# Kernel tuning notes

Hardware: AMD Instinct MI355X
Metric: run time of the kernel (lower is better)

The kernel has to match this reference:

```python
import jax, jax.numpy as jnp
import numpy as np

BETA = 4.0  # temperature of soft cluster assignment in filling loss


def _pairwise_sq_dist(a, b):
    # a: [N,D], b: [K,D] -> [N,K] squared euclidean distances
    return (jnp.sum(a * a, -1, keepdims=True)
            - 2.0 * (a @ b.T)
            + jnp.sum(b * b, -1)[None, :])


def setup_inputs() -> dict:
    key = jax.random.key(0)
    k1, k2, k3, k4 = jax.random.split(key, 4)
    N, D, K = 131072, 64, 16
    x = jax.random.normal(k1, (N, D), jnp.float32)
    cluster_centers = jax.random.normal(k2, (K, D), jnp.float32)
    target = jax.random.normal(k3, (N, D), jnp.float32)
    ft = jax.random.uniform(k4, (K,), jnp.float32)
    filling_target = ft / ft.sum()
    # prediction = kmeans assignment of the fixed target set (computed once, constant)
    prediction = jnp.argmin(_pairwise_sq_dist(target, cluster_centers), axis=-1)
    return {"x": x, "cluster_centers": cluster_centers,
            "filling_target": filling_target, "target": target,
            "prediction": prediction}


def reference(x, cluster_centers, filling_target, target, prediction):
    N, D = x.shape
    Nt = target.shape[0]
    K = cluster_centers.shape[0]
    BIG = jnp.finfo(x.dtype).max  # padding value that sorts to the end

    d2 = _pairwise_sq_dist(x, cluster_centers)  # [N,K]

    # --- cluster filling MSE: soft assignment fractions vs filling_target ---
    soft = jax.nn.softmax(-BETA * d2, axis=-1)          # [N,K]
    filling = soft.mean(axis=0)                          # [K]
    loss_fil = jnp.mean((filling - filling_target) ** 2)

    # --- per-cluster sorted (per-dimension 1D) Wasserstein distance ---
    pred_x = jax.lax.stop_gradient(jnp.argmin(d2, axis=-1))  # kmeans_predict(x).detach()
    L = min(N, Nt)  # static upper bound on per-cluster min_size
    rows = jnp.arange(L)

    loss_med = jnp.zeros((), x.dtype)
    for k in range(K):  # fixed structural loop over clusters
        mx = pred_x == k
        mt = prediction == k
        m = jnp.minimum(mx.sum(), mt.sum())  # min_size (dynamic value, static shapes)
        # keep only the FIRST m members (original order), as x[in_cluster][:m]
        keep_x = mx & ((jnp.cumsum(mx) - 1) < m)
        keep_t = mt & ((jnp.cumsum(mt) - 1) < m)
        # mask out non-members with BIG so they sort to the bottom, sort per dim
        xs = jnp.sort(jnp.where(keep_x[:, None], x, BIG), axis=0)[:L]       # [L,D]
        ts = jnp.sort(jnp.where(keep_t[:, None], target, BIG), axis=0)[:L]  # [L,D]
        valid = (rows < m)[:, None]                                          # [L,1]
        diff = jnp.where(valid, jnp.abs(xs - ts), 0.0)
        # mean(|sort(x) - sort(y)|) over the m x D selected elements
        denom = (m * D).astype(x.dtype)
        loss_med = loss_med + jnp.where(m > 0, diff.sum() / denom, 0.0)

    return loss_fil + loss_med
```

## Files before the change

### kernel.cpp

```cpp
#include <hip/hip_runtime.h>
#include <stdint.h>

#define N_ROWS 131072
#define DIMS 64
#define KCL 16
#define BETA 4.0f
#define NBLK 512
#define CHUNK 16384
#define STH 1024
#define SEG_STRIDE 263168
#define VOFF (1u<<21)

typedef unsigned long long u64;
typedef unsigned int u32;

__device__ __forceinline__ u32 enc_f(float f) {
  u32 u = __float_as_uint(f);
  return (u & 0x80000000u) ? ~u : (u | 0x80000000u);
}
__device__ __forceinline__ float dec_f(u32 e) {
  u32 u = (e & 0x80000000u) ? (e & 0x7FFFFFFFu) : ~e;
  return __uint_as_float(u);
}
__device__ __forceinline__ u32 U4(u32 u) { return u ^ ((u >> 3) & 7u); }

#define CS(a,b,dd) { u32 _mn = min(a,b), _mx = max(a,b); a = (dd)?_mn:_mx; b = (dd)?_mx:_mn; }
#define CSV(A,B,D) { CS(A.x,B.x,D) CS(A.y,B.y,D) CS(A.z,B.z,D) CS(A.w,B.w,D) }

#define M16G(a,b,c,d,e,f,g,h,i2,j2,k2,l,m,n,o,p,D) \
  CS(a,i2,D) CS(b,j2,D) CS(c,k2,D) CS(d,l,D) CS(e,m,D) CS(f,n,D) CS(g,o,D) CS(h,p,D) \
  CS(a,e,D)  CS(b,f,D)  CS(c,g,D)  CS(d,h,D) CS(i2,m,D) CS(j2,n,D) CS(k2,o,D) CS(l,p,D) \
  CS(a,c,D)  CS(b,d,D)  CS(e,g,D)  CS(f,h,D) CS(i2,k2,D) CS(j2,l,D) CS(m,o,D) CS(n,p,D) \
  CS(a,b,D)  CS(c,d,D)  CS(e,f,D)  CS(g,h,D) CS(i2,j2,D) CS(k2,l,D) CS(m,n,D) CS(o,p,D)

#define SORT16G(a,b,c,d,e,f,g,h,i2,j2,k2,l,m,n,o,p,D) \
  CS(a,b,D) CS(c,d,!(D)) CS(e,f,D) CS(g,h,!(D)) CS(i2,j2,D) CS(k2,l,!(D)) CS(m,n,D) CS(o,p,!(D)) \
  CS(a,c,D) CS(b,d,D) CS(e,g,!(D)) CS(f,h,!(D)) CS(i2,k2,D) CS(j2,l,D) CS(m,o,!(D)) CS(n,p,!(D)) \
  CS(a,b,D) CS(c,d,D) CS(e,f,!(D)) CS(g,h,!(D)) CS(i2,j2,D) CS(k2,l,D) CS(m,n,!(D)) CS(o,p,!(D)) \
  CS(a,e,D) CS(b,f,D) CS(c,g,D) CS(d,h,D) CS(i2,m,!(D)) CS(j2,n,!(D)) CS(k2,o,!(D)) CS(l,p,!(D)) \
  CS(a,c,D) CS(b,d,D) CS(e,g,D) CS(f,h,D) CS(i2,k2,!(D)) CS(j2,l,!(D)) CS(m,o,!(D)) CS(n,p,!(D)) \
  CS(a,b,D) CS(c,d,D) CS(e,f,D) CS(g,h,D) CS(i2,j2,!(D)) CS(k2,l,!(D)) CS(m,n,!(D)) CS(o,p,!(D)) \
  M16G(a,b,c,d,e,f,g,h,i2,j2,k2,l,m,n,o,p,D)

#define MERGE16F(D) M16G(r0,r1,r2,r3,r4,r5,r6,r7,r8,r9,r10,r11,r12,r13,r14,r15,D)
#define SORT16F(D)  SORT16G(r0,r1,r2,r3,r4,r5,r6,r7,r8,r9,r10,r11,r12,r13,r14,r15,D)

#define LOADTILE16(src) \
  { uint4 _a0=src[U4(ub+0)],_a1=src[U4(ub+1)],_a2=src[U4(ub+2)],_a3=src[U4(ub+3)]; \
    r0=_a0.x;r1=_a0.y;r2=_a0.z;r3=_a0.w; r4=_a1.x;r5=_a1.y;r6=_a1.z;r7=_a1.w; \
    r8=_a2.x;r9=_a2.y;r10=_a2.z;r11=_a2.w; r12=_a3.x;r13=_a3.y;r14=_a3.z;r15=_a3.w; }

#define STORETILE16(dst) \
  { dst[U4(ub+0)]=make_uint4(r0,r1,r2,r3);   dst[U4(ub+1)]=make_uint4(r4,r5,r6,r7); \
    dst[U4(ub+2)]=make_uint4(r8,r9,r10,r11); dst[U4(ub+3)]=make_uint4(r12,r13,r14,r15); }

__device__ __forceinline__ void wave_tail(uint4* lds4, u32 RU, u32 Lw, u32 gbase,
                                          u32 k, u32 jtop, u32 lane)
{
  u32 j = jtop;
  while (j >= 32u) {
    u32 ud = j >> 3;
    if (lane < (Lw >> 4)) {
      u32 bu = RU + (((lane & ~(ud - 1u)) << 2) | (lane & (ud - 1u)));
      bool up = (((gbase + (bu << 2)) & k) == 0u);
      uint4 A0 = lds4[U4(bu)],           A1 = lds4[U4(bu + ud)],
            A2 = lds4[U4(bu + 2u * ud)], A3 = lds4[U4(bu + 3u * ud)];
      CSV(A0,A2,up) CSV(A1,A3,up)
      CSV(A0,A1,up) CSV(A2,A3,up)
      lds4[U4(bu)] = A0;           lds4[U4(bu + ud)] = A1;
      lds4[U4(bu + 2u * ud)] = A2; lds4[U4(bu + 3u * ud)] = A3;
    }
    j >>= 2;
  }
  if (j == 16u) {
    u32 total = Lw >> 3;
    for (u32 inst = lane; inst < total; inst += 64u) {
      u32 bu = RU + (((inst & ~3u) << 1) | (inst & 3u));
      bool up = (((gbase + (bu << 2)) & k) == 0u);
      uint4 A = lds4[U4(bu)], B = lds4[U4(bu + 4u)];
      CSV(A,B,up)
      lds4[U4(bu)] = A; lds4[U4(bu + 4u)] = B;
    }
  }
}

__device__ __forceinline__ void cross1(uint4* lds4, u32 Wn, u32 gb, u32 k, u32 jtop, u32 tid)
{
  u32 ud = jtop >> 2;
  u32 total = Wn >> 3;
  for (u32 inst = tid; inst < total; inst += STH) {
    u32 bu = ((inst & ~(ud - 1u)) << 1) | (inst & (ud - 1u));
    bool up = (((gb + (bu << 2)) & k) == 0u);
    uint4 A = lds4[U4(bu)], B = lds4[U4(bu + ud)];
    CSV(A,B,up)
    lds4[U4(bu)] = A; lds4[U4(bu + ud)] = B;
  }
}
__device__ __forceinline__ void cross2(uint4* lds4, u32 Wn, u32 gb, u32 k, u32 jtop, u32 tid)
{
  u32 ud = jtop >> 3;
  u32 total = Wn >> 4;
  for (u32 inst = tid; inst < total; inst += STH) {
    u32 bu = ((inst & ~(ud - 1u)) << 2) | (inst & (ud - 1u));
    bool up = (((gb + (bu << 2)) & k) == 0u);
    uint4 A0 = lds4[U4(bu)],            A1 = lds4[U4(bu + ud)],
          A2 = lds4[U4(bu + 2u * ud)],  A3 = lds4[U4(bu + 3u * ud)];
    CSV(A0,A2,up) CSV(A1,A3,up)
    CSV(A0,A1,up) CSV(A2,A3,up)
    lds4[U4(bu)] = A0;           lds4[U4(bu + ud)] = A1;
    lds4[U4(bu + 2u * ud)] = A2; lds4[U4(bu + 3u * ud)] = A3;
  }
}
__device__ __forceinline__ void cross3(uint4* lds4, u32 Wn, u32 gb, u32 k, u32 jtop, u32 tid)
{
  u32 ud = jtop >> 4;
  u32 total = Wn >> 5;
  for (u32 inst = tid; inst < total; inst += STH) {
    u32 bu = ((inst & ~(ud - 1u)) << 3) | (inst & (ud - 1u));
    bool up = (((gb + (bu << 2)) & k) == 0u);
    uint4 A0 = lds4[U4(bu)],            A1 = lds4[U4(bu + ud)],
          A2 = lds4[U4(bu + 2u * ud)],  A3 = lds4[U4(bu + 3u * ud)],
          A4 = lds4[U4(bu + 4u * ud)],  A5 = lds4[U4(bu + 5u * ud)],
          A6 = lds4[U4(bu + 6u * ud)],  A7 = lds4[U4(bu + 7u * ud)];
    CSV(A0,A4,up) CSV(A1,A5,up) CSV(A2,A6,up) CSV(A3,A7,up)
    CSV(A0,A2,up) CSV(A1,A3,up) CSV(A4,A6,up) CSV(A5,A7,up)
    CSV(A0,A1,up) CSV(A2,A3,up) CSV(A4,A5,up) CSV(A6,A7,up)
    lds4[U4(bu)] = A0;           lds4[U4(bu + ud)] = A1;
    lds4[U4(bu + 2u * ud)] = A2; lds4[U4(bu + 3u * ud)] = A3;
    lds4[U4(bu + 4u * ud)] = A4; lds4[U4(bu + 5u * ud)] = A5;
    lds4[U4(bu + 6u * ud)] = A6; lds4[U4(bu + 7u * ud)] = A7;
  }
}

__global__ __launch_bounds__(256) void k_assign(
    const float* __restrict__ x, const float* __restrict__ centers,
    const int* __restrict__ predT, int* __restrict__ predX,
    float* __restrict__ fill_sum, u32* __restrict__ histX, u32* __restrict__ histT)
{
  __shared__ float c[KCL][DIMS];
  __shared__ float cn[KCL];
  __shared__ float fs[KCL];
  __shared__ u32 hx[KCL], ht[KCL];
  int tid = threadIdx.x;
  for (int t = tid; t < KCL * DIMS; t += 256) c[t / DIMS][t % DIMS] = centers[t];
  if (tid < KCL) { fs[tid] = 0.f; hx[tid] = 0; ht[tid] = 0; }
  __syncthreads();
  if (tid < KCL) {
    float s = 0.f;
    for (int d = 0; d < DIMS; ++d) s += c[tid][d] * c[tid][d];
    cn[tid] = s;
  }
  __syncthreads();
  int i = blockIdx.x * 256 + tid;
  const float4* xr = (const float4*)(x + (size_t)i * DIMS);
  float dot[KCL];
#pragma unroll
  for (int k = 0; k < KCL; ++k) dot[k] = 0.f;
  for (int t = 0; t < DIMS / 4; ++t) {
    float4 v = xr[t];
#pragma unroll
    for (int k = 0; k < KCL; ++k)
      dot[k] += v.x * c[k][4 * t] + v.y * c[k][4 * t + 1] + v.z * c[k][4 * t + 2] + v.w * c[k][4 * t + 3];
  }
  float sc[KCL];
  float smin = 3.0e38f; int kmin = 0;
#pragma unroll
  for (int k = 0; k < KCL; ++k) {
    sc[k] = cn[k] - 2.f * dot[k];
    if (sc[k] < smin) { smin = sc[k]; kmin = k; }
  }
  float e[KCL]; float esum = 0.f;
#pragma unroll
  for (int k = 0; k < KCL; ++k) { e[k] = expf(-BETA * (sc[k] - smin)); esum += e[k]; }
  float inv = 1.f / esum;
#pragma unroll
  for (int k = 0; k < KCL; ++k) atomicAdd(&fs[k], e[k] * inv);
  predX[i] = kmin;
  atomicAdd(&hx[kmin], 1u);
  atomicAdd(&ht[predT[i]], 1u);
  __syncthreads();
  if (tid < KCL) {
    histX[blockIdx.x * KCL + tid] = hx[tid];
    histT[blockIdx.x * KCL + tid] = ht[tid];
    atomicAdd(&fill_sum[tid], fs[tid]);
  }
}

__global__ __launch_bounds__(512) void k_scan(
    const u32* __restrict__ histX, const u32* __restrict__ histT,
    u32* __restrict__ baseX, u32* __restrict__ baseT,
    const float* __restrict__ fill_sum, const float* __restrict__ ftarget,
    int* __restrict__ m_out, float* __restrict__ w_out,
    int* __restrict__ p_out, int* __restrict__ pOff_out, int* __restrict__ mOff_out,
    int* __restrict__ nlo_out, float* __restrict__ loss_fil)
{
  __shared__ u32 part[2][KCL][17];
  __shared__ u32 tot[2][KCL];
  __shared__ float sq[KCL];
  __shared__ int sp[KCL];
  __shared__ int smv[KCL];
  int tid = threadIdx.x;
  int side = tid >> 8;
  int rem = tid & 255;
  int c = rem >> 4;
  int sub = rem & 15;
  const u32* hist = side ? histT : histX;
  u32* base = side ? baseT : baseX;
  int b0 = sub * 32;
  u32 s = 0;
  for (int b = b0; b < b0 + 32; ++b) s += hist[b * KCL + c];
  part[side][c][sub] = s;
  __syncthreads();
  if (sub == 0) {
    u32 run = 0;
    for (int t = 0; t < 16; ++t) { u32 v = part[side][c][t]; part[side][c][t] = run; run += v; }
    tot[side][c] = run;
  }
  __syncthreads();
  u32 run = part[side][c][sub];
  for (int b = b0; b < b0 + 32; ++b) { base[b * KCL + c] = run; run += hist[b * KCL + c]; }
  if (tid < KCL) {
    int m = min((int)tot[0][tid], (int)tot[1][tid]);
    m_out[tid] = m;
    smv[tid] = m;
    w_out[tid] = (m > 0) ? 1.f / ((float)m * (float)DIMS) : 0.f;
    int pp = 32;
    while (pp < m) pp <<= 1;
    sp[tid] = pp;
    p_out[tid] = pp;
    int nlo = 0;
    if (pp > CHUNK) {
      int nch = pp / CHUNK;
      for (int j = 1; j < nch; j += 2) {
        int v = m - j * CHUNK;
        if (v < 0) v = 0;
        if (v > CHUNK) v = CHUNK;
        nlo += CHUNK - v;
      }
    }
    nlo_out[tid] = nlo;
    float d = fill_sum[tid] / (float)N_ROWS - ftarget[tid];
    sq[tid] = d * d;
  }
  __syncthreads();
  if (tid == 0) {
    float s2 = 0.f;
    int acc = 0, macc = 0;
    for (int k = 0; k < KCL; ++k) {
      s2 += sq[k];
      pOff_out[k] = acc;
      acc += sp[k];
      mOff_out[k] = macc;
      macc += smv[k];
    }
    pOff_out[KCL] = acc;
    mOff_out[KCL] = macc;
    *loss_fil = s2 / (float)KCL;
  }
}

__global__ __launch_bounds__(256) void k_rank(
    const int* __restrict__ predX, const int* __restrict__ predT,
    const u32* __restrict__ baseX, const u32* __restrict__ baseT,
    const int* __restrict__ mG, const int* __restrict__ mOffG,
    int* __restrict__ idxX, int* __restrict__ idxT)
{
  __shared__ int wcX[4][KCL], wcT[4][KCL];
  __shared__ int smo[KCL], sm2[KCL];
  int tid = threadIdx.x;
  int lane = tid & 63, wave = tid >> 6;
  if (tid < KCL) { smo[tid] = mOffG[tid]; sm2[tid] = mG[tid]; }
  int i = blockIdx.x * 256 + tid;
  int kx = predX[i], kt = predT[i];
  u64 below = (1ull << lane) - 1ull;
  int lrX = 0, lrT = 0;
  for (int cc = 0; cc < KCL; ++cc) {
    u64 mx = __ballot(kx == cc);
    u64 mt = __ballot(kt == cc);
    if (kx == cc) lrX = __popcll(mx & below);
    if (kt == cc) lrT = __popcll(mt & below);
    if (lane == 0) { wcX[wave][cc] = __popcll(mx); wcT[wave][cc] = __popcll(mt); }
  }
  __syncthreads();
  int wbX = 0, wbT = 0;
  for (int w2 = 0; w2 < wave; ++w2) { wbX += wcX[w2][kx]; wbT += wcT[w2][kt]; }
  int rX = (int)baseX[blockIdx.x * KCL + kx] + wbX + lrX;
  int rT = (int)baseT[blockIdx.x * KCL + kt] + wbT + lrT;
  if (rX < sm2[kx]) idxX[smo[kx] + rX] = i;
  if (rT < sm2[kt]) idxT[smo[kt] + rT] = i;
}

__global__ __launch_bounds__(256) void k_gather(
    const float* __restrict__ x, const float* __restrict__ tgt,
    const int* __restrict__ idxX, const int* __restrict__ idxT,
    const int* __restrict__ pOffG, const int* __restrict__ mOffG,
    const int* __restrict__ mG, const int* __restrict__ pG,
    u32* __restrict__ valX, u32* __restrict__ valT, int d0, int Dbc)
{
  __shared__ int spOff[KCL + 1];
  __shared__ int smo[KCL], sm2[KCL], sp2[KCL];
  int tid = threadIdx.x;
  if (tid <= KCL) spOff[tid] = pOffG[tid];
  if (tid < KCL) { smo[tid] = mOffG[tid]; sm2[tid] = mG[tid]; sp2[tid] = pG[tid]; }
  __syncthreads();
  int pos = blockIdx.x * 256 + tid;
  if (pos >= spOff[KCL]) return;
  int c = 0;
#pragma unroll
  for (int cc = 1; cc < KCL; ++cc) c += (pos >= spOff[cc]) ? 1 : 0;
  int rel = pos - spOff[c];
  u32* dx = valX + pos;
  u32* dt = valT + pos;
  if (rel < sm2[c]) {
    int w = smo[c] + rel;
    int iX = idxX[w], iT = idxT[w];
    if ((Dbc & 3) == 0) {
      const float4* xr = (const float4*)(x + (size_t)iX * DIMS + d0);
      const float4* tr = (const float4*)(tgt + (size_t)iT * DIMS + d0);
      for (int q = 0; q < (Dbc >> 2); ++q) {
        float4 a = xr[q];
        float4 b = tr[q];
        size_t base = (size_t)(4 * q) * SEG_STRIDE;
        dx[base]                  = enc_f(a.x);
        dx[base + SEG_STRIDE]     = enc_f(a.y);
        dx[base + 2 * (size_t)SEG_STRIDE] = enc_f(a.z);
        dx[base + 3 * (size_t)SEG_STRIDE] = enc_f(a.w);
        dt[base]                  = enc_f(b.x);
        dt[base + SEG_STRIDE]     = enc_f(b.y);
        dt[base + 2 * (size_t)SEG_STRIDE] = enc_f(b.z);
        dt[base + 3 * (size_t)SEG_STRIDE] = enc_f(b.w);
      }
    } else {
      const float* xr = x + (size_t)iX * DIMS + d0;
      const float* tr = tgt + (size_t)iT * DIMS + d0;
      for (int d = 0; d < Dbc; ++d) {
        dx[(size_t)d * SEG_STRIDE] = enc_f(xr[d]);
        dt[(size_t)d * SEG_STRIDE] = enc_f(tr[d]);
      }
    }
  } else {
    u32 pv = (sp2[c] > CHUNK && ((rel >> 14) & 1)) ? 0u : 0xFFFFFFFFu;
    for (int d = 0; d < Dbc; ++d) {
      dx[(size_t)d * SEG_STRIDE] = pv;
      dt[(size_t)d * SEG_STRIDE] = pv;
    }
  }
}

__global__ __launch_bounds__(STH, 8) void k_sort(
    u32* __restrict__ vbase, const int* __restrict__ pG, const int* __restrict__ pOffG,
    const int* __restrict__ mG)
{
  __shared__ __align__(16) u32 lds[CHUNK];
  uint4* lds4 = (uint4*)lds;
  int t = blockIdx.x, c = -1, sub = 0, acc = 0;
  for (int cc = 0; cc < KCL; ++cc) {
    int pc0 = pG[cc];
    int nc = (pc0 > CHUNK) ? (pc0 / CHUNK) : 1;
    if (t < acc + nc) { c = cc; sub = t - acc; break; }
    acc += nc;
  }
  if (c < 0) return;
  int pc = pG[c];
  u32 CH = (u32)min(pc, CHUNK);
  u32 gb = (u32)sub * (u32)CHUNK;
  int v = mG[c] - (int)gb;
  if (v > (int)CH) v = (int)CH;
  if (v <= 0) return;
  u32 W = 32u;
  while (W < (u32)v) W <<= 1;
  if (W > CH) W = CH;
  bool desc = (pc > CHUNK) && (sub & 1);
  u32 inv = desc ? 0xFFFFFFFFu : 0u;
  u32* seg = vbase + (size_t)blockIdx.y * SEG_STRIDE + pOffG[c] + gb;
  uint4* gp4 = (uint4*)seg;
  u32 tid = threadIdx.x;
  u32 lane = tid & 63u;
  u32 wv = tid >> 6;
  u32 ub = tid << 2;
  u32 bas = tid << 4;
  bool act = (bas < W);
  u32 RU = wv << 8;
  u32 runBase = wv << 10;
  bool wact = (runBase < W);
  u32 Lw = W - runBase; if (Lw > 1024u) Lw = 1024u;
  u32 r0,r1,r2,r3,r4,r5,r6,r7,r8,r9,r10,r11,r12,r13,r14,r15;

  if (act) {
    uint4 a0 = gp4[ub + 0], a1 = gp4[ub + 1], a2 = gp4[ub + 2], a3 = gp4[ub + 3];
    r0 = a0.x^inv; r1 = a0.y^inv; r2  = a0.z^inv; r3  = a0.w^inv;
    r4 = a1.x^inv; r5 = a1.y^inv; r6  = a1.z^inv; r7  = a1.w^inv;
    r8 = a2.x^inv; r9 = a2.y^inv; r10 = a2.z^inv; r11 = a2.w^inv;
    r12 = a3.x^inv; r13 = a3.y^inv; r14 = a3.z^inv; r15 = a3.w^inv;
    bool D = ((bas & 16u) == 0u);
    SORT16F(D);
    STORETILE16(lds4);
  }
  if (wact) {
    for (u32 k = 32u; k <= Lw; k <<= 1) {
      wave_tail(lds4, RU, Lw, 0u, k, k >> 1, lane);
      if (act) {
        LOADTILE16(lds4);
        bool D = ((bas & k) == 0u);
        MERGE16F(D);
        if (k < W) { STORETILE16(lds4); }
        else {
          gp4[ub + 0] = make_uint4(r0^inv, r1^inv, r2^inv, r3^inv);
          gp4[ub + 1] = make_uint4(r4^inv, r5^inv, r6^inv, r7^inv);
          gp4[ub + 2] = make_uint4(r8^inv, r9^inv, r10^inv, r11^inv);
          gp4[ub + 3] = make_uint4(r12^inv, r13^inv, r14^inv, r15^inv);
        }
      }
    }
  }

  if (W >= 2048u) {
    __syncthreads();
    for (u32 k = 2048u; k <= W; k <<= 1) {
      u32 jt = k >> 1;
      if (jt >= 8192u) {
        cross3(lds4, W, 0u, k, 8192u, tid);
        __syncthreads();
        cross1(lds4, W, 0u, k, 1024u, tid);
        __syncthreads();
      } else if (jt == 4096u) {
        cross3(lds4, W, 0u, k, 4096u, tid);
        __syncthreads();
      } else if (jt == 2048u) {
        cross2(lds4, W, 0u, k, 2048u, tid);
        __syncthreads();
      } else {
        cross1(lds4, W, 0u, k, 1024u, tid);
        __syncthreads();
      }
      if (wact) {
        wave_tail(lds4, RU, Lw, 0u, k, 512u, lane);
        if (act) {
          LOADTILE16(lds4);
          bool D = ((bas & k) == 0u);
          MERGE16F(D);
          if (k < W) { STORETILE16(lds4); }
          else {
            gp4[ub + 0] = make_uint4(r0^inv, r1^inv, r2^inv, r3^inv);
            gp4[ub + 1] = make_uint4(r4^inv, r5^inv, r6^inv, r7^inv);
            gp4[ub + 2] = make_uint4(r8^inv, r9^inv, r10^inv, r11^inv);
            gp4[ub + 3] = make_uint4(r12^inv, r13^inv, r14^inv, r15^inv);
          }
        }
      }
      if (k < W) __syncthreads();
    }
  }
}

__global__ __launch_bounds__(256) void k_gpass(
    u32* __restrict__ vbase, const int* __restrict__ pG, const int* __restrict__ pOffG,
    int kk, int j)
{
  u32* base = vbase + (size_t)blockIdx.y * SEG_STRIDE;
  int pb[KCL]; int tot = 0;
#pragma unroll
  for (int c = 0; c < KCL; ++c) {
    pb[c] = tot;
    int pc = pG[c];
    if (pc >= kk) tot += pc >> 1;
  }
  for (int g4 = (blockIdx.x * 256 + threadIdx.x) << 2; g4 < tot; g4 += gridDim.x * 256 * 4) {
    int c = 0;
#pragma unroll
    for (int cc = 1; cc < KCL; ++cc) c += (g4 >= pb[cc]) ? 1 : 0;
    int u = g4 - pb[c];
    int i = ((u & ~(j - 1)) << 1) | (u & (j - 1));
    bool up = ((i & kk) == 0);
    u32* s2 = base + pOffG[c];
    uint4 A = *(const uint4*)(s2 + i);
    uint4 B = *(const uint4*)(s2 + i + j);
    CS(A.x, B.x, up) CS(A.y, B.y, up) CS(A.z, B.z, up) CS(A.w, B.w, up)
    *(uint4*)(s2 + i) = A;
    *(uint4*)(s2 + i + j) = B;
  }
}

__global__ __launch_bounds__(STH, 8) void k_gfinish(
    u32* __restrict__ vbase, const int* __restrict__ pG, const int* __restrict__ pOffG, int kk)
{
  __shared__ __align__(16) u32 lds[CHUNK];
  uint4* lds4 = (uint4*)lds;
  int t = blockIdx.x, c = -1, sub = 0, acc = 0;
  for (int cc = 0; cc < KCL; ++cc) {
    int pc = pG[cc];
    if (pc < kk) continue;
    int nc = pc / CHUNK;
    if (t < acc + nc) { c = cc; sub = t - acc; break; }
    acc += nc;
  }
  if (c < 0) return;
  u32 gb = (u32)sub * (u32)CHUNK;
  u32* seg = vbase + (size_t)blockIdx.y * SEG_STRIDE + pOffG[c] + gb;
  uint4* gp4 = (uint4*)seg;
  u32 tid = threadIdx.x;
  u32 lane = tid & 63u;
  u32 wv = tid >> 6;
  u32 RU = wv << 8;
  u32 ub = tid << 2;
  u32 bas = tid << 4;
  u32 r0,r1,r2,r3,r4,r5,r6,r7,r8,r9,r10,r11,r12,r13,r14,r15;

  for (u32 uu = tid; uu < CHUNK / 4; uu += STH) lds4[U4(uu)] = gp4[uu];
  __syncthreads();
  cross3(lds4, (u32)CHUNK, gb, (u32)kk, 8192u, tid);
  __syncthreads();
  cross1(lds4, (u32)CHUNK, gb, (u32)kk, 1024u, tid);
  __syncthreads();
  wave_tail(lds4, RU, 1024u, gb, (u32)kk, 512u, lane);
  {
    LOADTILE16(lds4);
    bool up = (((gb + bas) & (u32)kk) == 0u);
    MERGE16F(up);
    gp4[ub + 0] = make_uint4(r0, r1, r2, r3);
    gp4[ub + 1] = make_uint4(r4, r5, r6, r7);
    gp4[ub + 2] = make_uint4(r8, r9, r10, r11);
    gp4[ub + 3] = make_uint4(r12, r13, r14, r15);
  }
}

__global__ __launch_bounds__(256) void k_reduce(
    const u32* __restrict__ valX, const u32* __restrict__ valT,
    const int* __restrict__ pOffG, const int* __restrict__ mOffG,
    const int* __restrict__ nloG,
    const float* __restrict__ wG, float* __restrict__ lossAcc)
{
  __shared__ int spOff[KCL];
  __shared__ int smo[KCL + 1];
  __shared__ int snlo[KCL];
  __shared__ float swt[KCL];
  __shared__ float red[256];
  int tid = threadIdx.x;
  if (tid <= KCL) smo[tid] = mOffG[tid];
  if (tid < KCL) { spOff[tid] = pOffG[tid]; snlo[tid] = nloG[tid]; swt[tid] = wG[tid]; }
  __syncthreads();
  int d = blockIdx.y;
  const u32* vx = valX + (size_t)d * SEG_STRIDE;
  const u32* vt = valT + (size_t)d * SEG_STRIDE;
  int M = smo[KCL];
  float s = 0.f;
  for (int w = blockIdx.x * 256 + tid; w < M; w += gridDim.x * 256) {
    int c = 0;
#pragma unroll
    for (int cc = 1; cc < KCL; ++cc) c += (w >= smo[cc]) ? 1 : 0;
    int pos = spOff[c] + snlo[c] + (w - smo[c]);
    float a = dec_f(vx[pos]), b = dec_f(vt[pos]);
    s += fabsf(a - b) * swt[c];
  }
  red[tid] = s;
  __syncthreads();
  for (int st = 128; st > 0; st >>= 1) {
    if (tid < st) red[tid] += red[tid + st];
    __syncthreads();
  }
  if (tid == 0) atomicAdd(lossAcc, red[0]);
}

__global__ void k_final(const float* __restrict__ lossAcc, const float* __restrict__ loss_fil,
                        float* __restrict__ out)
{
  out[0] = *lossAcc + *loss_fil;
}

extern "C" void kernel_launch(void* const* d_in, const int* in_sizes, int n_in,
                              void* d_out, int out_size, void* d_ws, size_t ws_size,
                              hipStream_t stream)
{
  const float* x       = (const float*)d_in[0];
  const float* centers = (const float*)d_in[1];
  const float* ftarget = (const float*)d_in[2];
  const float* tgt     = (const float*)d_in[3];
  const int*   predT   = (const int*)d_in[4];
  float* out = (float*)d_out;

  char* ws = (char*)d_ws;
  float* fill_sum = (float*)(ws + 0);
  float* lossAcc  = (float*)(ws + 64);
  float* loss_fil = (float*)(ws + 68);
  int*   m_buf    = (int*)(ws + 128);
  float* w_buf    = (float*)(ws + 192);
  int*   p_buf    = (int*)(ws + 256);
  int*   pOff     = (int*)(ws + 320);
  int*   mOff     = (int*)(ws + 400);
  u32* histX = (u32*)(ws + 512);
  u32* histT = (u32*)(ws + 512 + 32768);
  u32* baseX = (u32*)(ws + 512 + 65536);
  u32* baseT = (u32*)(ws + 512 + 98304);
  int* predX = (int*)(ws + 131584);
  int* idxX  = (int*)(ws + 655872);
  int* idxT  = (int*)(ws + 1180160);
  int* nlo_buf = (int*)(ws + 1704448);
  u32* vbase = (u32*)(ws + VOFF);

  size_t avail_elems = (ws_size > VOFF) ? ((ws_size - VOFF) / 4) : 0;
  int Db = (int)(avail_elems / (2ull * SEG_STRIDE));
  if (Db > DIMS) Db = DIMS;
  if (Db >= 4) Db &= ~3;
  if (Db < 1) Db = 1;

  hipMemsetAsync(ws, 0, 128, stream);
  k_assign<<<NBLK, 256, 0, stream>>>(x, centers, predT, predX, fill_sum, histX, histT);
  k_scan<<<1, 512, 0, stream>>>(histX, histT, baseX, baseT, fill_sum, ftarget,
                                m_buf, w_buf, p_buf, pOff, mOff, nlo_buf, loss_fil);
  k_rank<<<NBLK, 256, 0, stream>>>(predX, predT, baseX, baseT, m_buf, mOff, idxX, idxT);

  for (int d0 = 0; d0 < DIMS; d0 += Db) {
    int Dbc = (Db < DIMS - d0) ? Db : (DIMS - d0);
    u32* valX = vbase;
    u32* valT = vbase + (size_t)Dbc * SEG_STRIDE;
    k_gather<<<1028, 256, 0, stream>>>(x, tgt, idxX, idxT, pOff, mOff, m_buf, p_buf,
                                       valX, valT, d0, Dbc);
    k_sort<<<dim3(26, 2 * Dbc), STH, 0, stream>>>(vbase, p_buf, pOff, m_buf);
    for (int kk = 2 * CHUNK; kk <= N_ROWS; kk <<= 1) {
      for (int j = kk >> 1; j >= CHUNK; j >>= 1)
        k_gpass<<<dim3(16, 2 * Dbc), 256, 0, stream>>>(vbase, p_buf, pOff, kk, j);
      k_gfinish<<<dim3(16, 2 * Dbc), STH, 0, stream>>>(vbase, p_buf, pOff, kk);
    }
    k_reduce<<<dim3(32, Dbc), 256, 0, stream>>>(valX, valT, pOff, mOff, nlo_buf,
                                                w_buf, lossAcc);
  }
  k_final<<<1, 1, 0, stream>>>(lossAcc, loss_fil, out);
}
```

Baseline: 652.8 us.

## Fuse global bitonic merge passes into one cooperative kernel with grid sync

Replaces the host loop of many small k_gpass/k_gfinish launches with one cooperative kernel that walks every global merge stage, using grid.sync between passes. It also changes the local sort's final write-back to go through LDS as a coalesced copy instead of per-thread tile stores, and gfinish likewise stages results in LDS before writing out. The aim is to remove per-launch overhead and tail idling across the many small passes. In exchange, the grid is capped at 256 blocks of 1024 threads, it depends on cooperative-launch residency, and it adds extra LDS round trips.

Measured after the change: 738.9 us. +13.2%, slower.

```diff
diff --git a/kernel.cpp b/kernel.cpp
--- a/kernel.cpp
+++ b/kernel.cpp
@@ -1,5 +1,8 @@
 #include <hip/hip_runtime.h>
+#include <hip/hip_cooperative_groups.h>
 #include <stdint.h>
+
+namespace cg = cooperative_groups;
 
 #define N_ROWS 131072
 #define DIMS 64
@@ -403,13 +406,7 @@
         LOADTILE16(lds4);
         bool D = ((bas & k) == 0u);
         MERGE16F(D);
-        if (k < W) { STORETILE16(lds4); }
-        else {
-          gp4[ub + 0] = make_uint4(r0^inv, r1^inv, r2^inv, r3^inv);
-          gp4[ub + 1] = make_uint4(r4^inv, r5^inv, r6^inv, r7^inv);
-          gp4[ub + 2] = make_uint4(r8^inv, r9^inv, r10^inv, r11^inv);
-          gp4[ub + 3] = make_uint4(r12^inv, r13^inv, r14^inv, r15^inv);
-        }
+        STORETILE16(lds4);
       }
     }
   }
@@ -439,88 +436,98 @@
           LOADTILE16(lds4);
           bool D = ((bas & k) == 0u);
           MERGE16F(D);
-          if (k < W) { STORETILE16(lds4); }
-          else {
-            gp4[ub + 0] = make_uint4(r0^inv, r1^inv, r2^inv, r3^inv);
-            gp4[ub + 1] = make_uint4(r4^inv, r5^inv, r6^inv, r7^inv);
-            gp4[ub + 2] = make_uint4(r8^inv, r9^inv, r10^inv, r11^inv);
-            gp4[ub + 3] = make_uint4(r12^inv, r13^inv, r14^inv, r15^inv);
-          }
+          STORETILE16(lds4);
         }
       }
       if (k < W) __syncthreads();
     }
   }
-}
-
-__global__ __launch_bounds__(256) void k_gpass(
-    u32* __restrict__ vbase, const int* __restrict__ pG, const int* __restrict__ pOffG,
-    int kk, int j)
-{
-  u32* base = vbase + (size_t)blockIdx.y * SEG_STRIDE;
-  int pb[KCL]; int tot = 0;
-#pragma unroll
-  for (int c = 0; c < KCL; ++c) {
-    pb[c] = tot;
-    int pc = pG[c];
-    if (pc >= kk) tot += pc >> 1;
-  }
-  for (int g4 = (blockIdx.x * 256 + threadIdx.x) << 2; g4 < tot; g4 += gridDim.x * 256 * 4) {
-    int c = 0;
-#pragma unroll
-    for (int cc = 1; cc < KCL; ++cc) c += (g4 >= pb[cc]) ? 1 : 0;
-    int u = g4 - pb[c];
-    int i = ((u & ~(j - 1)) << 1) | (u & (j - 1));
-    bool up = ((i & kk) == 0);
-    u32* s2 = base + pOffG[c];
-    uint4 A = *(const uint4*)(s2 + i);
-    uint4 B = *(const uint4*)(s2 + i + j);
-    CS(A.x, B.x, up) CS(A.y, B.y, up) CS(A.z, B.z, up) CS(A.w, B.w, up)
-    *(uint4*)(s2 + i) = A;
-    *(uint4*)(s2 + i + j) = B;
-  }
-}
-
-__global__ __launch_bounds__(STH, 8) void k_gfinish(
-    u32* __restrict__ vbase, const int* __restrict__ pG, const int* __restrict__ pOffG, int kk)
+
+  __syncthreads();
+  for (u32 uu = tid; (uu << 2) < W; uu += STH) {
+    uint4 q = lds4[U4(uu)];
+    q.x ^= inv; q.y ^= inv; q.z ^= inv; q.w ^= inv;
+    gp4[uu] = q;
+  }
+}
+
+__global__ __launch_bounds__(STH) void k_gbig(
+    u32* __restrict__ vbase, const int* __restrict__ pG,
+    const int* __restrict__ pOffG, int nplanes)
 {
   __shared__ __align__(16) u32 lds[CHUNK];
   uint4* lds4 = (uint4*)lds;
-  int t = blockIdx.x, c = -1, sub = 0, acc = 0;
-  for (int cc = 0; cc < KCL; ++cc) {
-    int pc = pG[cc];
-    if (pc < kk) continue;
-    int nc = pc / CHUNK;
-    if (t < acc + nc) { c = cc; sub = t - acc; break; }
-    acc += nc;
-  }
-  if (c < 0) return;
-  u32 gb = (u32)sub * (u32)CHUNK;
-  u32* seg = vbase + (size_t)blockIdx.y * SEG_STRIDE + pOffG[c] + gb;
-  uint4* gp4 = (uint4*)seg;
+  int p[KCL], pO[KCL];
+  int pmax = 0;
+#pragma unroll
+  for (int c = 0; c < KCL; ++c) {
+    p[c] = pG[c]; pO[c] = pOffG[c];
+    pmax = max(pmax, p[c]);
+  }
+  if (pmax <= CHUNK) return;
+  cg::grid_group grid = cg::this_grid();
   u32 tid = threadIdx.x;
-  u32 lane = tid & 63u;
-  u32 wv = tid >> 6;
-  u32 RU = wv << 8;
-  u32 ub = tid << 2;
-  u32 bas = tid << 4;
-  u32 r0,r1,r2,r3,r4,r5,r6,r7,r8,r9,r10,r11,r12,r13,r14,r15;
-
-  for (u32 uu = tid; uu < CHUNK / 4; uu += STH) lds4[U4(uu)] = gp4[uu];
-  __syncthreads();
-  cross3(lds4, (u32)CHUNK, gb, (u32)kk, 8192u, tid);
-  __syncthreads();
-  cross1(lds4, (u32)CHUNK, gb, (u32)kk, 1024u, tid);
-  __syncthreads();
-  wave_tail(lds4, RU, 1024u, gb, (u32)kk, 512u, lane);
-  {
-    LOADTILE16(lds4);
-    bool up = (((gb + bas) & (u32)kk) == 0u);
-    MERGE16F(up);
-    gp4[ub + 0] = make_uint4(r0, r1, r2, r3);
-    gp4[ub + 1] = make_uint4(r4, r5, r6, r7);
-    gp4[ub + 2] = make_uint4(r8, r9, r10, r11);
-    gp4[ub + 3] = make_uint4(r12, r13, r14, r15);
+  u32 lane = tid & 63u, wv = tid >> 6, RU = wv << 8, ub = tid << 2, bas = tid << 4;
+
+  for (int kk = 2 * CHUNK; kk <= N_ROWS; kk <<= 1) {
+    if (pmax < kk) break;
+    for (int j = kk >> 1; j >= CHUNK; j >>= 1) {
+      int pb[KCL]; int tot = 0;
+#pragma unroll
+      for (int c = 0; c < KCL; ++c) { pb[c] = tot; if (p[c] >= kk) tot += p[c] >> 3; }
+      long total = (long)tot * nplanes;
+      long gthr = (long)gridDim.x * STH;
+      for (long g = (long)blockIdx.x * STH + tid; g < total; g += gthr) {
+        int plane = (int)(g / tot);
+        int u4i = (int)(g % tot);
+        int c = 0;
+#pragma unroll
+        for (int cc = 1; cc < KCL; ++cc) c += (u4i >= pb[cc]) ? 1 : 0;
+        int u = (u4i - pb[c]) << 2;
+        int i = ((u & ~(j - 1)) << 1) | (u & (j - 1));
+        bool up = ((i & kk) == 0);
+        u32* s2 = vbase + (size_t)plane * SEG_STRIDE + pO[c];
+        uint4 A = *(const uint4*)(s2 + i);
+        uint4 B = *(const uint4*)(s2 + i + j);
+        CS(A.x, B.x, up) CS(A.y, B.y, up) CS(A.z, B.z, up) CS(A.w, B.w, up)
+        *(uint4*)(s2 + i) = A;
+        *(uint4*)(s2 + i + j) = B;
+      }
+      grid.sync();
+    }
+    int cb[KCL]; int nch = 0;
+#pragma unroll
+    for (int c = 0; c < KCL; ++c) { cb[c] = nch; if (p[c] >= kk) nch += p[c] / CHUNK; }
+    int totc = nch * nplanes;
+    for (int item = blockIdx.x; item < totc; item += gridDim.x) {
+      int plane = item / nch;
+      int ch = item % nch;
+      int c = 0;
+#pragma unroll
+      for (int cc = 1; cc < KCL; ++cc) c += (ch >= cb[cc]) ? 1 : 0;
+      int sub = ch - cb[c];
+      u32 gb = (u32)sub * (u32)CHUNK;
+      u32* seg = vbase + (size_t)plane * SEG_STRIDE + pO[c] + gb;
+      uint4* gp4 = (uint4*)seg;
+      for (u32 uu = tid; uu < CHUNK / 4; uu += STH) lds4[U4(uu)] = gp4[uu];
+      __syncthreads();
+      cross3(lds4, (u32)CHUNK, gb, (u32)kk, 8192u, tid);
+      __syncthreads();
+      cross1(lds4, (u32)CHUNK, gb, (u32)kk, 1024u, tid);
+      __syncthreads();
+      wave_tail(lds4, RU, 1024u, gb, (u32)kk, 512u, lane);
+      {
+        u32 r0,r1,r2,r3,r4,r5,r6,r7,r8,r9,r10,r11,r12,r13,r14,r15;
+        LOADTILE16(lds4);
+        bool up = (((gb + bas) & (u32)kk) == 0u);
+        MERGE16F(up);
+        STORETILE16(lds4);
+      }
+      __syncthreads();
+      for (u32 uu = tid; uu < CHUNK / 4; uu += STH) gp4[uu] = lds4[U4(uu)];
+      __syncthreads();
+    }
+    grid.sync();
   }
 }
 
@@ -616,10 +623,14 @@
     k_gather<<<1028, 256, 0, stream>>>(x, tgt, idxX, idxT, pOff, mOff, m_buf, p_buf,
                                        valX, valT, d0, Dbc);
     k_sort<<<dim3(26, 2 * Dbc), STH, 0, stream>>>(vbase, p_buf, pOff, m_buf);
-    for (int kk = 2 * CHUNK; kk <= N_ROWS; kk <<= 1) {
-      for (int j = kk >> 1; j >= CHUNK; j >>= 1)
-        k_gpass<<<dim3(16, 2 * Dbc), 256, 0, stream>>>(vbase, p_buf, pOff, kk, j);
-      k_gfinish<<<dim3(16, 2 * Dbc), STH, 0, stream>>>(vbase, p_buf, pOff, kk);
+    {
+      u32* vb = vbase;
+      const int* pb = p_buf;
+      const int* po = pOff;
+      int np = 2 * Dbc;
+      void* gargs[] = { (void*)&vb, (void*)&pb, (void*)&po, (void*)&np };
+      hipLaunchCooperativeKernel((const void*)k_gbig, dim3(256), dim3(STH),
+                                 gargs, 0, stream);
     }
     k_reduce<<<dim3(32, Dbc), 256, 0, stream>>>(valX, valT, pOff, mOff, nlo_buf,
                                                 w_buf, lossAcc);
```
